# Kernel optimization log

Measured on AMD Instinct MI355X. Metric: run time of the kernel, lower is better.

Reference implementation:

```python
import jax, jax.numpy as jnp
import numpy as np

N, E, F_IN, F_HID, K = 100000, 1600000, 64, 64, 6


def setup_inputs() -> dict:
    key = jax.random.key(0)
    k1, k2, k3, k4, k5 = jax.random.split(key, 5)
    x = jax.random.normal(k1, (N, F_IN), dtype=jnp.float32)
    # edges with no self-loops (PyG ChebConv removes self loops before normalization)
    src = jax.random.randint(k2, (E,), 0, N, dtype=jnp.int32)
    off = jax.random.randint(k3, (E,), 1, N, dtype=jnp.int32)
    dst = (src + off) % N
    edge_index = jnp.stack([src, dst], axis=0)
    # Glorot-ish init for the K Chebyshev weight matrices
    W = jax.random.normal(k4, (K, F_IN, F_HID), dtype=jnp.float32) * (1.0 / np.sqrt(F_IN))
    b = jax.random.normal(k5, (F_HID,), dtype=jnp.float32) * 0.01
    return {"x": x, "edge_index": edge_index, "W": W, "b": b}


def reference(x, edge_index, W, b):
    # ChebConv with sym normalization, lambda_max = 2.0 (PyG default):
    # scaled Laplacian L_hat = 2*L/lambda_max - I = -D^{-1/2} A D^{-1/2} (zero diagonal)
    row = edge_index[0].astype(jnp.int32)  # source j
    col = edge_index[1].astype(jnp.int32)  # target i
    n = x.shape[0]
    deg = jax.ops.segment_sum(jnp.ones_like(row, dtype=x.dtype), row, num_segments=n)
    dinv = jnp.where(deg > 0, jax.lax.rsqrt(deg), jnp.zeros_like(deg))
    w = -(dinv[row] * dinv[col])  # [E] edge weights of L_hat

    def prop(h):  # h: [N, F] -> L_hat @ h via gather-scale-scatter
        return jax.ops.segment_sum(w[:, None] * h[row], col, num_segments=n)

    # Chebyshev recurrence: Tx_0 = x, Tx_1 = L_hat x, Tx_k = 2 L_hat Tx_{k-1} - Tx_{k-2}
    Tx0 = x
    out = Tx0 @ W[0]
    Tx1 = prop(Tx0)
    out = out + Tx1 @ W[1]
    for k in range(2, W.shape[0]):
        Tx2 = 2.0 * prop(Tx1) - Tx0
        out = out + Tx2 @ W[k]
        Tx0, Tx1 = Tx1, Tx2
    return jax.nn.relu(out + b)
```

## Files before the change

kernel.cpp:

```cpp
#include <hip/hip_runtime.h>


constexpr int F = 64;
constexpr int SCAN_ELEMS = 1024;
constexpr int BSH = 9;
constexpr int EPB = 2048;
constexpr int PNPW = 8;

typedef __attribute__((ext_vector_type(8))) short short8;
typedef __attribute__((ext_vector_type(4))) float floatx4;
typedef __attribute__((ext_vector_type(2))) float floatx2;

#if defined(__has_builtin)
#if __has_builtin(__builtin_amdgcn_cvt_pk_f32_fp8) && __has_builtin(__builtin_amdgcn_cvt_pk_fp8_f32)
#define HAVE_FP8 1
#endif
#endif
#ifndef HAVE_FP8
#define HAVE_FP8 0
#endif

__device__ __forceinline__ unsigned short f_to_bf(float f) {
    unsigned u = __float_as_uint(f);
    u += 0x7FFFu + ((u >> 16) & 1u);
    return (unsigned short)(u >> 16);
}
__device__ __forceinline__ float bf_to_f(unsigned short s) {
    return __uint_as_float(((unsigned)s) << 16);
}
__device__ __forceinline__ float4 bf4_to_f4(ushort4 u) {
    float4 f;
    f.x = bf_to_f(u.x); f.y = bf_to_f(u.y); f.z = bf_to_f(u.z); f.w = bf_to_f(u.w);
    return f;
}

#if HAVE_FP8
__device__ __forceinline__ float4 fp8x4_to_f4(unsigned u) {
    floatx2 lo = __builtin_amdgcn_cvt_pk_f32_fp8((int)u, false);
    floatx2 hi = __builtin_amdgcn_cvt_pk_f32_fp8((int)u, true);
    float4 f;
    f.x = lo.x; f.y = lo.y; f.z = hi.x; f.w = hi.y;
    return f;
}
__device__ __forceinline__ unsigned f4_to_fp8x4(float a, float b, float c, float d) {
    int pk = 0;
    pk = __builtin_amdgcn_cvt_pk_fp8_f32(a, b, pk, false);
    pk = __builtin_amdgcn_cvt_pk_fp8_f32(c, d, pk, true);
    return (unsigned)pk;
}
#else
__device__ __forceinline__ float4 fp8x4_to_f4(unsigned u) { return make_float4(0, 0, 0, 0); }
__device__ __forceinline__ unsigned f4_to_fp8x4(float a, float b, float c, float d) { return 0; }
#endif

__global__ void hist2_kernel(const int* __restrict__ row, const int* __restrict__ col,
                             int* __restrict__ gcH, int* __restrict__ gcS,
                             int P, int G, int E) {
    __shared__ int hH[256], hS[256];
    const int tid = threadIdx.x, blk = blockIdx.x;
    hH[tid] = 0; hS[tid] = 0;
    __syncthreads();
    const int start = blk * EPB + tid * 8;
    if (start + 7 < E) {
        const int4 c0 = *(const int4*)(col + start);
        const int4 c1 = *(const int4*)(col + start + 4);
        const int4 r0 = *(const int4*)(row + start);
        const int4 r1 = *(const int4*)(row + start + 4);
        atomicAdd(&hH[c0.x >> BSH], 1); atomicAdd(&hH[c0.y >> BSH], 1);
        atomicAdd(&hH[c0.z >> BSH], 1); atomicAdd(&hH[c0.w >> BSH], 1);
        atomicAdd(&hH[c1.x >> BSH], 1); atomicAdd(&hH[c1.y >> BSH], 1);
        atomicAdd(&hH[c1.z >> BSH], 1); atomicAdd(&hH[c1.w >> BSH], 1);
        atomicAdd(&hS[r0.x >> BSH], 1); atomicAdd(&hS[r0.y >> BSH], 1);
        atomicAdd(&hS[r0.z >> BSH], 1); atomicAdd(&hS[r0.w >> BSH], 1);
        atomicAdd(&hS[r1.x >> BSH], 1); atomicAdd(&hS[r1.y >> BSH], 1);
        atomicAdd(&hS[r1.z >> BSH], 1); atomicAdd(&hS[r1.w >> BSH], 1);
    } else {
        for (int k = start; k < E && k < start + 8; ++k) {
            atomicAdd(&hH[col[k] >> BSH], 1);
            atomicAdd(&hS[row[k] >> BSH], 1);
        }
    }
    __syncthreads();
    if (tid < P) {
        gcH[(size_t)tid * G + blk] = hH[tid];
        gcS[(size_t)tid * G + blk] = hS[tid];
    }
}

__device__ __forceinline__ int4 load_cnt4(const int* __restrict__ cnt, int i, int N) {
    int4 v = make_int4(0, 0, 0, 0);
    if (i + 3 < N) {
        v = *(const int4*)(cnt + i);
    } else {
        if (i + 0 < N) v.x = cnt[i + 0];
        if (i + 1 < N) v.y = cnt[i + 1];
        if (i + 2 < N) v.z = cnt[i + 2];
        if (i + 3 < N) v.w = cnt[i + 3];
    }
    return v;
}

__global__ void scan1_kernel(const int* __restrict__ cnt, int* __restrict__ bsum, int N) {
    const int tid = threadIdx.x;
    const int i = blockIdx.x * SCAN_ELEMS + tid * 4;
    int4 v = load_cnt4(cnt, i, N);
    int s = v.x + v.y + v.z + v.w;
#pragma unroll
    for (int off = 1; off < 64; off <<= 1) s += __shfl_xor(s, off);
    __shared__ int ws[4];
    if ((tid & 63) == 0) ws[tid >> 6] = s;
    __syncthreads();
    if (tid == 0) bsum[blockIdx.x] = ws[0] + ws[1] + ws[2] + ws[3];
}

__global__ void scan2_kernel(const int* __restrict__ bsum, int* __restrict__ boff,
                             int* __restrict__ total_out, int nb) {
    const int tid = threadIdx.x;
    const int lane = tid & 63, w = tid >> 6;
    int v = (tid < nb) ? bsum[tid] : 0;
    int inc = v;
#pragma unroll
    for (int off = 1; off < 64; off <<= 1) {
        int t = __shfl_up(inc, off);
        if (lane >= off) inc += t;
    }
    __shared__ int wsum[4];
    if (lane == 63) wsum[w] = inc;
    __syncthreads();
    int wo = 0;
    for (int k = 0; k < w; ++k) wo += wsum[k];
    const int excl = wo + inc - v;
    if (tid < nb) boff[tid] = excl;
    if (tid == nb - 1) *total_out = excl + v;
}

__global__ void scan3_kernel(const int* __restrict__ cnt, const int* __restrict__ boff,
                             int* __restrict__ dst, int N) {
    const int tid = threadIdx.x;
    const int lane = tid & 63, w = tid >> 6;
    const int i = blockIdx.x * SCAN_ELEMS + tid * 4;
    int4 v = load_cnt4(cnt, i, N);
    const int s = v.x + v.y + v.z + v.w;
    int inc = s;
#pragma unroll
    for (int off = 1; off < 64; off <<= 1) {
        int t = __shfl_up(inc, off);
        if (lane >= off) inc += t;
    }
    __shared__ int wsum[4];
    if (lane == 63) wsum[w] = inc;
    __syncthreads();
    int wo = 0;
    for (int k = 0; k < w; ++k) wo += wsum[k];
    const int r0 = boff[blockIdx.x] + wo + inc - s;
    const int r1 = r0 + v.x, r2 = r1 + v.y, r3 = r2 + v.z;
    if (i + 3 < N) {
        *(int4*)(dst + i) = make_int4(r0, r1, r2, r3);
    } else {
        if (i + 0 < N) dst[i + 0] = r0;
        if (i + 1 < N) dst[i + 1] = r1;
        if (i + 2 < N) dst[i + 2] = r2;
        if (i + 3 < N) dst[i + 3] = r3;
    }
}

__global__ void part2_kernel(const int* __restrict__ row, const int* __restrict__ col,
                             const int* __restrict__ goH, const int* __restrict__ goS,
                             int* __restrict__ partH, int* __restrict__ partS,
                             int P, int G, int E) {
    __shared__ int cH[256], cS[256];
    const int tid = threadIdx.x, blk = blockIdx.x;
    if (tid < P) {
        cH[tid] = goH[(size_t)tid * G + blk];
        cS[tid] = goS[(size_t)tid * G + blk];
    }
    __syncthreads();
    const int start = blk * EPB + tid * 8;
    for (int k = start; k < E && k < start + 8; ++k) {
        const int c = col[k], r = row[k];
        const int posH = atomicAdd(&cH[c >> BSH], 1);
        partH[posH] = ((c & ((1 << BSH) - 1)) << 23) | r;
        const int posS = atomicAdd(&cS[r >> BSH], 1);
        partS[posS] = r;
    }
}

__global__ void bucketC_kernel(const int* __restrict__ part, const int* __restrict__ goff,
                               int* __restrict__ rowptr, int* __restrict__ csr,
                               int P, int G, int N, int E) {
    __shared__ int cnt[512];
    __shared__ int excl[512];
    __shared__ int wsum[4];
    const int tid = threadIdx.x;
    const int b = blockIdx.x;
    const int base_node = b << BSH;
    const int nn = min(512, N - base_node);
    const int estart = goff[(size_t)b * G];
    const int eend = (b + 1 < P) ? goff[(size_t)(b + 1) * G] : E;

    cnt[tid] = 0; cnt[tid + 256] = 0;
    __syncthreads();
    for (int i = estart + tid; i < eend; i += 256)
        atomicAdd(&cnt[((unsigned)part[i]) >> 23], 1);
    __syncthreads();
    {
        const int lane = tid & 63, w = tid >> 6;
        const int a0 = cnt[2 * tid], a1 = cnt[2 * tid + 1];
        const int ps = a0 + a1;
        int inc = ps;
#pragma unroll
        for (int off = 1; off < 64; off <<= 1) {
            int t = __shfl_up(inc, off);
            if (lane >= off) inc += t;
        }
        if (lane == 63) wsum[w] = inc;
        __syncthreads();
        int wo = 0;
        for (int k = 0; k < w; ++k) wo += wsum[k];
        const int ep = wo + inc - ps;
        excl[2 * tid] = ep;
        excl[2 * tid + 1] = ep + a0;
    }
    __syncthreads();
    if (tid < nn) rowptr[base_node + tid] = estart + excl[tid];
    for (int ln = 256 + tid; ln < nn; ln += 256) rowptr[base_node + ln] = estart + excl[ln];
    if (b == P - 1 && tid == 0) rowptr[N] = E;
    cnt[tid] = 0; cnt[tid + 256] = 0;
    __syncthreads();
    for (int i = estart + tid; i < eend; i += 256) {
        const int pk = part[i];
        const int ln = ((unsigned)pk) >> 23;
        const int pos = atomicAdd(&cnt[ln], 1);
        csr[estart + excl[ln] + pos] = pk & 0x7FFFFF;
    }
}

__global__ void bucketD_kernel(const int* __restrict__ partS, const int* __restrict__ goffS,
                               float* __restrict__ dinv, float* __restrict__ dinv2,
                               float* __restrict__ rdinv, int P, int G, int N, int E) {
    __shared__ int cnt[512];
    const int tid = threadIdx.x;
    const int b = blockIdx.x;
    const int base_node = b << BSH;
    const int nn = min(512, N - base_node);
    const int estart = goffS[(size_t)b * G];
    const int eend = (b + 1 < P) ? goffS[(size_t)(b + 1) * G] : E;
    cnt[tid] = 0; cnt[tid + 256] = 0;
    __syncthreads();
    for (int i = estart + tid; i < eend; i += 256)
        atomicAdd(&cnt[partS[i] - base_node], 1);
    __syncthreads();
    for (int l = tid; l < nn; l += 256) {
        const int dI = cnt[l];
        const float d = (float)dI;
        const bool ok = dI > 0;
        dinv[base_node + l]  = ok ? rsqrtf(d) : 0.0f;
        dinv2[base_node + l] = ok ? 1.0f / d : 0.0f;
        rdinv[base_node + l] = ok ? sqrtf(d) : 0.0f;
    }
}

__global__ void init_s0_kernel(const float* __restrict__ dinv, const float* __restrict__ x,
                               unsigned short* __restrict__ S0b, unsigned char* __restrict__ S0f8,
                               int NF, int write8) {
    int i = blockIdx.x * blockDim.x + threadIdx.x;
    int j = i * 4;
    if (j >= NF) return;
    const float dv = dinv[j >> 6];
    const float4 v = *(const float4*)(x + j);
    const float a = dv * v.x, bb = dv * v.y, c = dv * v.z, d = dv * v.w;
    ushort4 u;
    u.x = f_to_bf(a); u.y = f_to_bf(bb); u.z = f_to_bf(c); u.w = f_to_bf(d);
    *(ushort4*)(S0b + j) = u;
    if (write8) *(unsigned*)(S0f8 + j) = f4_to_fp8x4(a, bb, c, d);
}

template <int FIRST>
__global__ __launch_bounds__(256, 6)
void prop_g4(const int* __restrict__ rowptr, const int* __restrict__ csr,
             const float* __restrict__ dinv2, const unsigned short* __restrict__ Sprev,
             const unsigned short* __restrict__ Sm2, unsigned short* __restrict__ Sk, int N) {
    const int lane = threadIdx.x & 63;
    const int g16 = lane & 48;
    const int fl = lane & 15;
    const int wave = threadIdx.x >> 6;
    const int wbase = (blockIdx.x * 4 + wave) * PNPW;
    for (int j = 0; j < PNPW; j += 4) {
        const int n = wbase + j + (g16 >> 4);
        const bool nv = n < N;
        const int nc = nv ? n : N - 1;
        const int s = rowptr[nc], e = rowptr[nc + 1];
        const int len = e - s;
        float4 acc = {0.f, 0.f, 0.f, 0.f};
        for (int c = 0; c < len; c += 16) {
            const int ii = s + c + fl;
            const int idxv = csr[ii < e ? ii : e - 1];
            const int mm = min(16, len - c);
            ushort4 u[16];
#pragma unroll
            for (int t = 0; t < 16; ++t) {
                const int it = __shfl(idxv, g16 + t);
                u[t] = *(const ushort4*)(Sprev + (size_t)it * F + fl * 4);
            }
#pragma unroll
            for (int t = 0; t < 16; ++t) {
                if (t < mm) {
                    const float4 v = bf4_to_f4(u[t]);
                    acc.x += v.x; acc.y += v.y; acc.z += v.z; acc.w += v.w;
                }
            }
        }
        if (nv) {
            const float d2 = dinv2[n];
            float4 sn;
            if (FIRST) {
                sn.x = -d2 * acc.x; sn.y = -d2 * acc.y;
                sn.z = -d2 * acc.z; sn.w = -d2 * acc.w;
            } else {
                const float4 m2 = bf4_to_f4(*(const ushort4*)(Sm2 + (size_t)n * F + fl * 4));
                sn.x = -2.f * d2 * acc.x - m2.x; sn.y = -2.f * d2 * acc.y - m2.y;
                sn.z = -2.f * d2 * acc.z - m2.z; sn.w = -2.f * d2 * acc.w - m2.w;
            }
            ushort4 o;
            o.x = f_to_bf(sn.x); o.y = f_to_bf(sn.y);
            o.z = f_to_bf(sn.z); o.w = f_to_bf(sn.w);
            *(ushort4*)(Sk + (size_t)n * F + fl * 4) = o;
        }
    }
}

template <int FIRST, int W8>
__global__ __launch_bounds__(256, 6)
void prop_f8(const int* __restrict__ rowptr, const int* __restrict__ csr,
             const float* __restrict__ dinv2, const unsigned char* __restrict__ S8prev,
             const unsigned short* __restrict__ Sm2, unsigned short* __restrict__ Sk,
             unsigned char* __restrict__ Sk8, int N) {
    const int lane = threadIdx.x & 63;
    const int g16 = lane & 48;
    const int fl = lane & 15;
    const int wave = threadIdx.x >> 6;
    const int wbase = (blockIdx.x * 4 + wave) * PNPW;
    for (int j = 0; j < PNPW; j += 4) {
        const int n = wbase + j + (g16 >> 4);
        const bool nv = n < N;
        const int nc = nv ? n : N - 1;
        const int s = rowptr[nc], e = rowptr[nc + 1];
        const int len = e - s;
        float4 acc = {0.f, 0.f, 0.f, 0.f};
        for (int c = 0; c < len; c += 16) {
            const int ii = s + c + fl;
            const int idxv = csr[ii < e ? ii : e - 1];
            const int mm = min(16, len - c);
            unsigned u[16];
#pragma unroll
            for (int t = 0; t < 16; ++t) {
                const int it = __shfl(idxv, g16 + t);
                u[t] = *(const unsigned*)(S8prev + (size_t)it * F + fl * 4);
            }
#pragma unroll
            for (int t = 0; t < 16; ++t) {
                if (t < mm) {
                    const float4 v = fp8x4_to_f4(u[t]);
                    acc.x += v.x; acc.y += v.y; acc.z += v.z; acc.w += v.w;
                }
            }
        }
        if (nv) {
            const float d2 = dinv2[n];
            float4 sn;
            if (FIRST) {
                sn.x = -d2 * acc.x; sn.y = -d2 * acc.y;
                sn.z = -d2 * acc.z; sn.w = -d2 * acc.w;
            } else {
                const float4 m2 = bf4_to_f4(*(const ushort4*)(Sm2 + (size_t)n * F + fl * 4));
                sn.x = -2.f * d2 * acc.x - m2.x; sn.y = -2.f * d2 * acc.y - m2.y;
                sn.z = -2.f * d2 * acc.z - m2.z; sn.w = -2.f * d2 * acc.w - m2.w;
            }
            ushort4 o;
            o.x = f_to_bf(sn.x); o.y = f_to_bf(sn.y);
            o.z = f_to_bf(sn.z); o.w = f_to_bf(sn.w);
            *(ushort4*)(Sk + (size_t)n * F + fl * 4) = o;
            if (W8) *(unsigned*)(Sk8 + (size_t)n * F + fl * 4) = f4_to_fp8x4(sn.x, sn.y, sn.z, sn.w);
        }
    }
}

__global__ void wfrag_kernel(const float* __restrict__ W, unsigned short* __restrict__ Wfrag) {
    const int idx = blockIdx.x * blockDim.x + threadIdx.x;
    if (idx >= 4 * 12 * 64) return;
    const int lane = idx & 63;
    const int s = (idx >> 6) % 12;
    const int ft = idx / (64 * 12);
    const int n = ft * 16 + (lane & 15);
    const int quad = lane >> 4;
    unsigned short v[8];
#pragma unroll
    for (int j = 0; j < 8; ++j) {
        const int kg = s * 32 + quad * 8 + j;
        const int kk = kg >> 6, f = kg & 63;
        v[j] = f_to_bf(W[kk * F * F + f * F + n]);
    }
    ushort4 lo = {v[0], v[1], v[2], v[3]};
    ushort4 hi = {v[4], v[5], v[6], v[7]};
    *(ushort4*)(Wfrag + (size_t)idx * 8) = lo;
    *(ushort4*)(Wfrag + (size_t)idx * 8 + 4) = hi;
}

__global__ __launch_bounds__(256, 3)
void mfma_out_kernel(const float* __restrict__ x, const unsigned short* __restrict__ Sstack,
                     const unsigned short* __restrict__ Wfrag, const float* __restrict__ rdinv,
                     const float* __restrict__ dinv2, const float* __restrict__ W,
                     const float* __restrict__ b, float* __restrict__ out, int N, int NF) {
    const int lane = threadIdx.x & 63;
    const int wave = threadIdx.x >> 6;
    const int quad = lane >> 4;
    const int fl = lane & 15;
    const int tm = (blockIdx.x * 4 + wave) * 16;
    if (tm >= N) return;
    const int ma = tm + fl;
    const int mac = ma < N ? ma : N - 1;

    const unsigned short* sa = Sstack + (size_t)mac * F + quad * 8;

    short8 Afr[12];
#pragma unroll
    for (int s = 0; s < 12; ++s) {
        const int kk = s >> 1, f0 = (s & 1) * 32;
        Afr[s] = *(const short8*)(sa + (size_t)kk * NF + f0);
    }

    floatx4 C0 = {0.f, 0.f, 0.f, 0.f};
    floatx4 C1 = {0.f, 0.f, 0.f, 0.f};
    floatx4 C2 = {0.f, 0.f, 0.f, 0.f};
    floatx4 C3 = {0.f, 0.f, 0.f, 0.f};
    const unsigned short* wf = Wfrag + (size_t)lane * 8;
#pragma unroll
    for (int s = 0; s < 12; ++s) {
        const short8 B0 = *(const short8*)(wf + (size_t)(0 * 12 + s) * 64 * 8);
        const short8 B1 = *(const short8*)(wf + (size_t)(1 * 12 + s) * 64 * 8);
        const short8 B2 = *(const short8*)(wf + (size_t)(2 * 12 + s) * 64 * 8);
        const short8 B3 = *(const short8*)(wf + (size_t)(3 * 12 + s) * 64 * 8);
        C0 = __builtin_amdgcn_mfma_f32_16x16x32_bf16(Afr[s], B0, C0, 0, 0, 0);
        C1 = __builtin_amdgcn_mfma_f32_16x16x32_bf16(Afr[s], B1, C1, 0, 0, 0);
        C2 = __builtin_amdgcn_mfma_f32_16x16x32_bf16(Afr[s], B2, C2, 0, 0, 0);
        C3 = __builtin_amdgcn_mfma_f32_16x16x32_bf16(Afr[s], B3, C3, 0, 0, 0);
    }

    const float bl0 = b[0 * 16 + fl];
    const float bl1 = b[1 * 16 + fl];
    const float bl2 = b[2 * 16 + fl];
    const float bl3 = b[3 * 16 + fl];

#pragma unroll
    for (int r = 0; r < 4; ++r) {
        const int m = tm + quad * 4 + r;
        if (m >= N) continue;
        const float rs = rdinv[m];
        const bool z = (dinv2[m] == 0.0f);
        float v0 = rs * C0[r], v1 = rs * C1[r], v2 = rs * C2[r], v3 = rs * C3[r];
        if (z) {
            const float* xr = x + (size_t)m * F;
            float f0 = 0.f, f1 = 0.f, f2 = 0.f, f3 = 0.f;
            for (int f = 0; f < F; ++f) {
                const float xv = xr[f];
                const float* w0 = W + 0 * F * F + f * F;
                const float* w2 = W + 2 * F * F + f * F;
                const float* w4 = W + 4 * F * F + f * F;
                f0 += xv * (w0[0 * 16 + fl] - w2[0 * 16 + fl] + w4[0 * 16 + fl]);
                f1 += xv * (w0[1 * 16 + fl] - w2[1 * 16 + fl] + w4[1 * 16 + fl]);
                f2 += xv * (w0[2 * 16 + fl] - w2[2 * 16 + fl] + w4[2 * 16 + fl]);
                f3 += xv * (w0[3 * 16 + fl] - w2[3 * 16 + fl] + w4[3 * 16 + fl]);
            }
            v0 = f0; v1 = f1; v2 = f2; v3 = f3;
        }
        float* orow = out + (size_t)m * F;
        orow[0 * 16 + fl] = fmaxf(v0 + bl0, 0.f);
        orow[1 * 16 + fl] = fmaxf(v1 + bl1, 0.f);
        orow[2 * 16 + fl] = fmaxf(v2 + bl2, 0.f);
        orow[3 * 16 + fl] = fmaxf(v3 + bl3, 0.f);
    }
}

extern "C" void kernel_launch(void* const* d_in, const int* in_sizes, int n_in,
                              void* d_out, int out_size, void* d_ws, size_t ws_size,
                              hipStream_t stream) {
    const float* x = (const float*)d_in[0];
    const int* ei = (const int*)d_in[1];
    const float* W = (const float*)d_in[2];
    const float* b = (const float*)d_in[3];

    const int N = in_sizes[0] / F;
    const int E = in_sizes[1] / 2;
    const int NF = N * F;
    const int* row = ei;
    const int* col = ei + E;

    const int P = (N + 511) >> BSH;
    const int G = (E + EPB - 1) / EPB;
    const int M = P * G;

    char* p = (char*)d_ws;
    auto alloc = [&](size_t bytes) {
        char* r = p;
        p += (bytes + 63) & ~(size_t)63;
        return r;
    };
    float* dinv   = (float*)alloc((size_t)N * sizeof(float));
    float* dinv2  = (float*)alloc((size_t)N * sizeof(float));
    float* rdinv  = (float*)alloc((size_t)N * sizeof(float));
    int*   rowptr = (int*)alloc((size_t)(N + 1) * sizeof(int));
    int*   bsum   = (int*)alloc(256 * sizeof(int));
    int*   boff   = (int*)alloc(256 * sizeof(int));
    int*   totS   = (int*)alloc(64);
    int*   gcH    = (int*)alloc((size_t)M * sizeof(int));
    int*   goH    = (int*)alloc((size_t)M * sizeof(int));
    int*   gcS    = (int*)alloc((size_t)M * sizeof(int));
    int*   goS    = (int*)alloc((size_t)M * sizeof(int));
    int*   csr    = (int*)alloc((size_t)E * sizeof(int));
    unsigned short* Sstack = (unsigned short*)alloc((size_t)6 * NF * sizeof(unsigned short));
    unsigned short* Wfrag  = (unsigned short*)alloc((size_t)4 * 12 * 64 * 8 * sizeof(unsigned short));
    unsigned char* F8A = (unsigned char*)alloc((size_t)NF);
    unsigned char* F8B = (unsigned char*)alloc((size_t)NF);
    const size_t needed = (size_t)(p - (char*)d_ws);
    const bool pathA = HAVE_FP8 && ws_size >= needed;
    int* partH = (int*)Sstack;
    int* partS = (int*)(Sstack + (size_t)NF);
    float* out = (float*)d_out;

    const int B = 256;
    const int nsbM = (M + SCAN_ELEMS - 1) / SCAN_ELEMS;
    const int pgrid = (N + 4 * PNPW - 1) / (4 * PNPW);

    hist2_kernel<<<G, B, 0, stream>>>(row, col, gcH, gcS, P, G, E);
    scan1_kernel<<<nsbM, B, 0, stream>>>(gcH, bsum, M);
    scan2_kernel<<<1, B, 0, stream>>>(bsum, boff, rowptr + N, nsbM);
    scan3_kernel<<<nsbM, B, 0, stream>>>(gcH, boff, goH, M);
    scan1_kernel<<<nsbM, B, 0, stream>>>(gcS, bsum, M);
    scan2_kernel<<<1, B, 0, stream>>>(bsum, boff, totS, nsbM);
    scan3_kernel<<<nsbM, B, 0, stream>>>(gcS, boff, goS, M);
    part2_kernel<<<G, B, 0, stream>>>(row, col, goH, goS, partH, partS, P, G, E);
    bucketC_kernel<<<P, B, 0, stream>>>(partH, goH, rowptr, csr, P, G, N, E);
    bucketD_kernel<<<P, B, 0, stream>>>(partS, goS, dinv, dinv2, rdinv, P, G, N, E);

    wfrag_kernel<<<(4 * 12 * 64 + B - 1) / B, B, 0, stream>>>(W, Wfrag);
    init_s0_kernel<<<(NF / 4 + B - 1) / B, B, 0, stream>>>(dinv, x, Sstack, F8A, NF,
                                                           pathA ? 1 : 0);
    unsigned short* S1 = Sstack + (size_t)1 * NF;
    unsigned short* S2 = Sstack + (size_t)2 * NF;
    unsigned short* S3 = Sstack + (size_t)3 * NF;
    unsigned short* S4 = Sstack + (size_t)4 * NF;
    unsigned short* S5 = Sstack + (size_t)5 * NF;
    if (pathA) {
        prop_f8<1, 1><<<pgrid, B, 0, stream>>>(rowptr, csr, dinv2, F8A, Sstack, S1, F8B, N);
        prop_f8<0, 1><<<pgrid, B, 0, stream>>>(rowptr, csr, dinv2, F8B, Sstack, S2, F8A, N);
        prop_f8<0, 1><<<pgrid, B, 0, stream>>>(rowptr, csr, dinv2, F8A, S1, S3, F8B, N);
        prop_f8<0, 1><<<pgrid, B, 0, stream>>>(rowptr, csr, dinv2, F8B, S2, S4, F8A, N);
        prop_f8<0, 0><<<pgrid, B, 0, stream>>>(rowptr, csr, dinv2, F8A, S3, S5, F8B, N);
    } else {
        prop_g4<1><<<pgrid, B, 0, stream>>>(rowptr, csr, dinv2, Sstack, Sstack, S1, N);
        prop_g4<0><<<pgrid, B, 0, stream>>>(rowptr, csr, dinv2, S1, Sstack, S2, N);
        prop_g4<0><<<pgrid, B, 0, stream>>>(rowptr, csr, dinv2, S2, S1, S3, N);
        prop_g4<0><<<pgrid, B, 0, stream>>>(rowptr, csr, dinv2, S3, S2, S4, N);
        prop_g4<0><<<pgrid, B, 0, stream>>>(rowptr, csr, dinv2, S4, S3, S5, N);
    }
    mfma_out_kernel<<<(N + 63) / 64, 256, 0, stream>>>(x, Sstack, Wfrag, rdinv, dinv2,
                                                       W, b, out, N, NF);
}
```

Baseline: 368.0 us.

## Merge graph preprocessing kernels and drop the FP8 propagation path

Several preprocessing stages are merged into fewer launches. The two histogram scans now run as one scan over a combined count array, the two bucket kernels become one launch, and the weight-fragment build is fused with the first feature scaling. The edge-partition loop now uses vectorized loads, and the output kernel uses nontemporal loads and stores. The FP8 gather path is removed, so all five propagation steps gather bf16 features. That cuts launch and sync overhead in the setup phase but doubles the bytes gathered per neighbour in the dominant propagation kernels.

```diff
diff --git a/kernel.cpp b/kernel.cpp
--- a/kernel.cpp
+++ b/kernel.cpp
@@ -2,23 +2,14 @@
 
 
 constexpr int F = 64;
-constexpr int SCAN_ELEMS = 1024;
+constexpr int SCAN_ELEMS = 2048;
 constexpr int BSH = 9;
 constexpr int EPB = 2048;
 constexpr int PNPW = 8;
+constexpr int WFRAG_BLOCKS = 12;
 
 typedef __attribute__((ext_vector_type(8))) short short8;
 typedef __attribute__((ext_vector_type(4))) float floatx4;
-typedef __attribute__((ext_vector_type(2))) float floatx2;
-
-#if defined(__has_builtin)
-#if __has_builtin(__builtin_amdgcn_cvt_pk_f32_fp8) && __has_builtin(__builtin_amdgcn_cvt_pk_fp8_f32)
-#define HAVE_FP8 1
-#endif
-#endif
-#ifndef HAVE_FP8
-#define HAVE_FP8 0
-#endif
 
 __device__ __forceinline__ unsigned short f_to_bf(float f) {
     unsigned u = __float_as_uint(f);
@@ -33,25 +24,6 @@
     f.x = bf_to_f(u.x); f.y = bf_to_f(u.y); f.z = bf_to_f(u.z); f.w = bf_to_f(u.w);
     return f;
 }
-
-#if HAVE_FP8
-__device__ __forceinline__ float4 fp8x4_to_f4(unsigned u) {
-    floatx2 lo = __builtin_amdgcn_cvt_pk_f32_fp8((int)u, false);
-    floatx2 hi = __builtin_amdgcn_cvt_pk_f32_fp8((int)u, true);
-    float4 f;
-    f.x = lo.x; f.y = lo.y; f.z = hi.x; f.w = hi.y;
-    return f;
-}
-__device__ __forceinline__ unsigned f4_to_fp8x4(float a, float b, float c, float d) {
-    int pk = 0;
-    pk = __builtin_amdgcn_cvt_pk_fp8_f32(a, b, pk, false);
-    pk = __builtin_amdgcn_cvt_pk_fp8_f32(c, d, pk, true);
-    return (unsigned)pk;
-}
-#else
-__device__ __forceinline__ float4 fp8x4_to_f4(unsigned u) { return make_float4(0, 0, 0, 0); }
-__device__ __forceinline__ unsigned f4_to_fp8x4(float a, float b, float c, float d) { return 0; }
-#endif
 
 __global__ void hist2_kernel(const int* __restrict__ row, const int* __restrict__ col,
                              int* __restrict__ gcH, int* __restrict__ gcS,
@@ -102,9 +74,10 @@
 
 __global__ void scan1_kernel(const int* __restrict__ cnt, int* __restrict__ bsum, int N) {
     const int tid = threadIdx.x;
-    const int i = blockIdx.x * SCAN_ELEMS + tid * 4;
-    int4 v = load_cnt4(cnt, i, N);
-    int s = v.x + v.y + v.z + v.w;
+    const int i = blockIdx.x * SCAN_ELEMS + tid * 8;
+    int4 va = load_cnt4(cnt, i, N);
+    int4 vb = load_cnt4(cnt, i + 4, N);
+    int s = va.x + va.y + va.z + va.w + vb.x + vb.y + vb.z + vb.w;
 #pragma unroll
     for (int off = 1; off < 64; off <<= 1) s += __shfl_xor(s, off);
     __shared__ int ws[4];
@@ -138,9 +111,10 @@
                              int* __restrict__ dst, int N) {
     const int tid = threadIdx.x;
     const int lane = tid & 63, w = tid >> 6;
-    const int i = blockIdx.x * SCAN_ELEMS + tid * 4;
-    int4 v = load_cnt4(cnt, i, N);
-    const int s = v.x + v.y + v.z + v.w;
+    const int i = blockIdx.x * SCAN_ELEMS + tid * 8;
+    int4 va = load_cnt4(cnt, i, N);
+    int4 vb = load_cnt4(cnt, i + 4, N);
+    const int s = va.x + va.y + va.z + va.w + vb.x + vb.y + vb.z + vb.w;
     int inc = s;
 #pragma unroll
     for (int off = 1; off < 64; off <<= 1) {
@@ -153,14 +127,21 @@
     int wo = 0;
     for (int k = 0; k < w; ++k) wo += wsum[k];
     const int r0 = boff[blockIdx.x] + wo + inc - s;
-    const int r1 = r0 + v.x, r2 = r1 + v.y, r3 = r2 + v.z;
+    const int r1 = r0 + va.x, r2 = r1 + va.y, r3 = r2 + va.z;
+    const int r4 = r3 + va.w, r5 = r4 + vb.x, r6 = r5 + vb.y, r7 = r6 + vb.z;
     if (i + 3 < N) {
         *(int4*)(dst + i) = make_int4(r0, r1, r2, r3);
     } else {
         if (i + 0 < N) dst[i + 0] = r0;
         if (i + 1 < N) dst[i + 1] = r1;
         if (i + 2 < N) dst[i + 2] = r2;
-        if (i + 3 < N) dst[i + 3] = r3;
+    }
+    if (i + 7 < N) {
+        *(int4*)(dst + i + 4) = make_int4(r4, r5, r6, r7);
+    } else {
+        if (i + 4 < N) dst[i + 4] = r4;
+        if (i + 5 < N) dst[i + 5] = r5;
+        if (i + 6 < N) dst[i + 6] = r6;
     }
 }
 
@@ -172,107 +153,145 @@
     const int tid = threadIdx.x, blk = blockIdx.x;
     if (tid < P) {
         cH[tid] = goH[(size_t)tid * G + blk];
-        cS[tid] = goS[(size_t)tid * G + blk];
+        cS[tid] = goS[(size_t)tid * G + blk] - E;
     }
     __syncthreads();
     const int start = blk * EPB + tid * 8;
-    for (int k = start; k < E && k < start + 8; ++k) {
-        const int c = col[k], r = row[k];
-        const int posH = atomicAdd(&cH[c >> BSH], 1);
-        partH[posH] = ((c & ((1 << BSH) - 1)) << 23) | r;
-        const int posS = atomicAdd(&cS[r >> BSH], 1);
-        partS[posS] = r;
-    }
-}
-
-__global__ void bucketC_kernel(const int* __restrict__ part, const int* __restrict__ goff,
-                               int* __restrict__ rowptr, int* __restrict__ csr,
-                               int P, int G, int N, int E) {
+    if (start + 7 < E) {
+        const int4 c0 = *(const int4*)(col + start);
+        const int4 c1 = *(const int4*)(col + start + 4);
+        const int4 r0 = *(const int4*)(row + start);
+        const int4 r1 = *(const int4*)(row + start + 4);
+#define P2_DO(c, r)                                              \
+        {                                                        \
+            const int posH = atomicAdd(&cH[(c) >> BSH], 1);      \
+            partH[posH] = (((c) & ((1 << BSH) - 1)) << 23) | (r);\
+            const int posS = atomicAdd(&cS[(r) >> BSH], 1);      \
+            partS[posS] = (r);                                   \
+        }
+        P2_DO(c0.x, r0.x) P2_DO(c0.y, r0.y) P2_DO(c0.z, r0.z) P2_DO(c0.w, r0.w)
+        P2_DO(c1.x, r1.x) P2_DO(c1.y, r1.y) P2_DO(c1.z, r1.z) P2_DO(c1.w, r1.w)
+#undef P2_DO
+    } else {
+        for (int k = start; k < E && k < start + 8; ++k) {
+            const int c = col[k], r = row[k];
+            const int posH = atomicAdd(&cH[c >> BSH], 1);
+            partH[posH] = ((c & ((1 << BSH) - 1)) << 23) | r;
+            const int posS = atomicAdd(&cS[r >> BSH], 1);
+            partS[posS] = r;
+        }
+    }
+}
+
+__global__ void bucketCD_kernel(const int* __restrict__ part, const int* __restrict__ goff,
+                                const int* __restrict__ partS, const int* __restrict__ goffS,
+                                int* __restrict__ rowptr, int* __restrict__ csr,
+                                float* __restrict__ dinv, float* __restrict__ dinv2,
+                                float* __restrict__ rdinv,
+                                int P, int G, int N, int E) {
     __shared__ int cnt[512];
     __shared__ int excl[512];
     __shared__ int wsum[4];
     const int tid = threadIdx.x;
-    const int b = blockIdx.x;
-    const int base_node = b << BSH;
-    const int nn = min(512, N - base_node);
-    const int estart = goff[(size_t)b * G];
-    const int eend = (b + 1 < P) ? goff[(size_t)(b + 1) * G] : E;
-
-    cnt[tid] = 0; cnt[tid + 256] = 0;
-    __syncthreads();
-    for (int i = estart + tid; i < eend; i += 256)
-        atomicAdd(&cnt[((unsigned)part[i]) >> 23], 1);
-    __syncthreads();
-    {
-        const int lane = tid & 63, w = tid >> 6;
-        const int a0 = cnt[2 * tid], a1 = cnt[2 * tid + 1];
-        const int ps = a0 + a1;
-        int inc = ps;
-#pragma unroll
-        for (int off = 1; off < 64; off <<= 1) {
-            int t = __shfl_up(inc, off);
-            if (lane >= off) inc += t;
-        }
-        if (lane == 63) wsum[w] = inc;
-        __syncthreads();
-        int wo = 0;
-        for (int k = 0; k < w; ++k) wo += wsum[k];
-        const int ep = wo + inc - ps;
-        excl[2 * tid] = ep;
-        excl[2 * tid + 1] = ep + a0;
-    }
-    __syncthreads();
-    if (tid < nn) rowptr[base_node + tid] = estart + excl[tid];
-    for (int ln = 256 + tid; ln < nn; ln += 256) rowptr[base_node + ln] = estart + excl[ln];
-    if (b == P - 1 && tid == 0) rowptr[N] = E;
-    cnt[tid] = 0; cnt[tid + 256] = 0;
-    __syncthreads();
-    for (int i = estart + tid; i < eend; i += 256) {
-        const int pk = part[i];
-        const int ln = ((unsigned)pk) >> 23;
-        const int pos = atomicAdd(&cnt[ln], 1);
-        csr[estart + excl[ln] + pos] = pk & 0x7FFFFF;
-    }
-}
-
-__global__ void bucketD_kernel(const int* __restrict__ partS, const int* __restrict__ goffS,
-                               float* __restrict__ dinv, float* __restrict__ dinv2,
-                               float* __restrict__ rdinv, int P, int G, int N, int E) {
-    __shared__ int cnt[512];
+    const int bb = blockIdx.x;
+    if (bb < P) {
+        const int b = bb;
+        const int base_node = b << BSH;
+        const int nn = min(512, N - base_node);
+        const int estart = goff[(size_t)b * G];
+        const int eend = (b + 1 < P) ? goff[(size_t)(b + 1) * G] : E;
+
+        cnt[tid] = 0; cnt[tid + 256] = 0;
+        __syncthreads();
+        for (int i = estart + tid; i < eend; i += 256)
+            atomicAdd(&cnt[((unsigned)part[i]) >> 23], 1);
+        __syncthreads();
+        {
+            const int lane = tid & 63, w = tid >> 6;
+            const int a0 = cnt[2 * tid], a1 = cnt[2 * tid + 1];
+            const int ps = a0 + a1;
+            int inc = ps;
+#pragma unroll
+            for (int off = 1; off < 64; off <<= 1) {
+                int t = __shfl_up(inc, off);
+                if (lane >= off) inc += t;
+            }
+            if (lane == 63) wsum[w] = inc;
+            __syncthreads();
+            int wo = 0;
+            for (int k = 0; k < w; ++k) wo += wsum[k];
+            const int ep = wo + inc - ps;
+            excl[2 * tid] = ep;
+            excl[2 * tid + 1] = ep + a0;
+        }
+        __syncthreads();
+        for (int ln = tid; ln < nn; ln += 256) rowptr[base_node + ln] = estart + excl[ln];
+        if (b == P - 1 && tid == 0) rowptr[N] = E;
+        cnt[tid] = 0; cnt[tid + 256] = 0;
+        __syncthreads();
+        for (int i = estart + tid; i < eend; i += 256) {
+            const int pk = part[i];
+            const int ln = ((unsigned)pk) >> 23;
+            const int pos = atomicAdd(&cnt[ln], 1);
+            csr[estart + excl[ln] + pos] = pk & 0x7FFFFF;
+        }
+    } else {
+        const int b = bb - P;
+        const int base_node = b << BSH;
+        const int nn = min(512, N - base_node);
+        const int estart = goffS[(size_t)b * G] - E;
+        const int eend = ((b + 1 < P) ? goffS[(size_t)(b + 1) * G] - E : E);
+        cnt[tid] = 0; cnt[tid + 256] = 0;
+        __syncthreads();
+        for (int i = estart + tid; i < eend; i += 256)
+            atomicAdd(&cnt[partS[i] - base_node], 1);
+        __syncthreads();
+        for (int l = tid; l < nn; l += 256) {
+            const int dI = cnt[l];
+            const float d = (float)dI;
+            const bool ok = dI > 0;
+            dinv[base_node + l]  = ok ? rsqrtf(d) : 0.0f;
+            dinv2[base_node + l] = ok ? 1.0f / d : 0.0f;
+            rdinv[base_node + l] = ok ? sqrtf(d) : 0.0f;
+        }
+    }
+}
+
+__global__ void init_ws0_kernel(const float* __restrict__ W, unsigned short* __restrict__ Wfrag,
+                                const float* __restrict__ dinv, const float* __restrict__ x,
+                                unsigned short* __restrict__ S0b, int NF) {
     const int tid = threadIdx.x;
-    const int b = blockIdx.x;
-    const int base_node = b << BSH;
-    const int nn = min(512, N - base_node);
-    const int estart = goffS[(size_t)b * G];
-    const int eend = (b + 1 < P) ? goffS[(size_t)(b + 1) * G] : E;
-    cnt[tid] = 0; cnt[tid + 256] = 0;
-    __syncthreads();
-    for (int i = estart + tid; i < eend; i += 256)
-        atomicAdd(&cnt[partS[i] - base_node], 1);
-    __syncthreads();
-    for (int l = tid; l < nn; l += 256) {
-        const int dI = cnt[l];
-        const float d = (float)dI;
-        const bool ok = dI > 0;
-        dinv[base_node + l]  = ok ? rsqrtf(d) : 0.0f;
-        dinv2[base_node + l] = ok ? 1.0f / d : 0.0f;
-        rdinv[base_node + l] = ok ? sqrtf(d) : 0.0f;
-    }
-}
-
-__global__ void init_s0_kernel(const float* __restrict__ dinv, const float* __restrict__ x,
-                               unsigned short* __restrict__ S0b, unsigned char* __restrict__ S0f8,
-                               int NF, int write8) {
-    int i = blockIdx.x * blockDim.x + threadIdx.x;
-    int j = i * 4;
-    if (j >= NF) return;
-    const float dv = dinv[j >> 6];
-    const float4 v = *(const float4*)(x + j);
-    const float a = dv * v.x, bb = dv * v.y, c = dv * v.z, d = dv * v.w;
-    ushort4 u;
-    u.x = f_to_bf(a); u.y = f_to_bf(bb); u.z = f_to_bf(c); u.w = f_to_bf(d);
-    *(ushort4*)(S0b + j) = u;
-    if (write8) *(unsigned*)(S0f8 + j) = f4_to_fp8x4(a, bb, c, d);
+    const int bid = blockIdx.x;
+    if (bid < WFRAG_BLOCKS) {
+        const int idx = bid * 256 + tid;
+        if (idx >= 4 * 12 * 64) return;
+        const int lane = idx & 63;
+        const int s = (idx >> 6) % 12;
+        const int ft = idx / (64 * 12);
+        const int n = ft * 16 + (lane & 15);
+        const int quad = lane >> 4;
+        unsigned short v[8];
+#pragma unroll
+        for (int j = 0; j < 8; ++j) {
+            const int kg = s * 32 + quad * 8 + j;
+            const int kk = kg >> 6, f = kg & 63;
+            v[j] = f_to_bf(W[kk * F * F + f * F + n]);
+        }
+        ushort4 lo = {v[0], v[1], v[2], v[3]};
+        ushort4 hi = {v[4], v[5], v[6], v[7]};
+        *(ushort4*)(Wfrag + (size_t)idx * 8) = lo;
+        *(ushort4*)(Wfrag + (size_t)idx * 8 + 4) = hi;
+    } else {
+        const int i = (bid - WFRAG_BLOCKS) * 256 + tid;
+        const int j = i * 4;
+        if (j >= NF) return;
+        const float dv = dinv[j >> 6];
+        const float4 v = *(const float4*)(x + j);
+        ushort4 u;
+        u.x = f_to_bf(dv * v.x); u.y = f_to_bf(dv * v.y);
+        u.z = f_to_bf(dv * v.z); u.w = f_to_bf(dv * v.w);
+        *(ushort4*)(S0b + j) = u;
+    }
 }
 
 template <int FIRST>
@@ -329,83 +348,6 @@
     }
 }
 
-template <int FIRST, int W8>
-__global__ __launch_bounds__(256, 6)
-void prop_f8(const int* __restrict__ rowptr, const int* __restrict__ csr,
-             const float* __restrict__ dinv2, const unsigned char* __restrict__ S8prev,
-             const unsigned short* __restrict__ Sm2, unsigned short* __restrict__ Sk,
-             unsigned char* __restrict__ Sk8, int N) {
-    const int lane = threadIdx.x & 63;
-    const int g16 = lane & 48;
-    const int fl = lane & 15;
-    const int wave = threadIdx.x >> 6;
-    const int wbase = (blockIdx.x * 4 + wave) * PNPW;
-    for (int j = 0; j < PNPW; j += 4) {
-        const int n = wbase + j + (g16 >> 4);
-        const bool nv = n < N;
-        const int nc = nv ? n : N - 1;
-        const int s = rowptr[nc], e = rowptr[nc + 1];
-        const int len = e - s;
-        float4 acc = {0.f, 0.f, 0.f, 0.f};
-        for (int c = 0; c < len; c += 16) {
-            const int ii = s + c + fl;
-            const int idxv = csr[ii < e ? ii : e - 1];
-            const int mm = min(16, len - c);
-            unsigned u[16];
-#pragma unroll
-            for (int t = 0; t < 16; ++t) {
-                const int it = __shfl(idxv, g16 + t);
-                u[t] = *(const unsigned*)(S8prev + (size_t)it * F + fl * 4);
-            }
-#pragma unroll
-            for (int t = 0; t < 16; ++t) {
-                if (t < mm) {
-                    const float4 v = fp8x4_to_f4(u[t]);
-                    acc.x += v.x; acc.y += v.y; acc.z += v.z; acc.w += v.w;
-                }
-            }
-        }
-        if (nv) {
-            const float d2 = dinv2[n];
-            float4 sn;
-            if (FIRST) {
-                sn.x = -d2 * acc.x; sn.y = -d2 * acc.y;
-                sn.z = -d2 * acc.z; sn.w = -d2 * acc.w;
-            } else {
-                const float4 m2 = bf4_to_f4(*(const ushort4*)(Sm2 + (size_t)n * F + fl * 4));
-                sn.x = -2.f * d2 * acc.x - m2.x; sn.y = -2.f * d2 * acc.y - m2.y;
-                sn.z = -2.f * d2 * acc.z - m2.z; sn.w = -2.f * d2 * acc.w - m2.w;
-            }
-            ushort4 o;
-            o.x = f_to_bf(sn.x); o.y = f_to_bf(sn.y);
-            o.z = f_to_bf(sn.z); o.w = f_to_bf(sn.w);
-            *(ushort4*)(Sk + (size_t)n * F + fl * 4) = o;
-            if (W8) *(unsigned*)(Sk8 + (size_t)n * F + fl * 4) = f4_to_fp8x4(sn.x, sn.y, sn.z, sn.w);
-        }
-    }
-}
-
-__global__ void wfrag_kernel(const float* __restrict__ W, unsigned short* __restrict__ Wfrag) {
-    const int idx = blockIdx.x * blockDim.x + threadIdx.x;
-    if (idx >= 4 * 12 * 64) return;
-    const int lane = idx & 63;
-    const int s = (idx >> 6) % 12;
-    const int ft = idx / (64 * 12);
-    const int n = ft * 16 + (lane & 15);
-    const int quad = lane >> 4;
-    unsigned short v[8];
-#pragma unroll
-    for (int j = 0; j < 8; ++j) {
-        const int kg = s * 32 + quad * 8 + j;
-        const int kk = kg >> 6, f = kg & 63;
-        v[j] = f_to_bf(W[kk * F * F + f * F + n]);
-    }
-    ushort4 lo = {v[0], v[1], v[2], v[3]};
-    ushort4 hi = {v[4], v[5], v[6], v[7]};
-    *(ushort4*)(Wfrag + (size_t)idx * 8) = lo;
-    *(ushort4*)(Wfrag + (size_t)idx * 8 + 4) = hi;
-}
-
 __global__ __launch_bounds__(256, 3)
 void mfma_out_kernel(const float* __restrict__ x, const unsigned short* __restrict__ Sstack,
                      const unsigned short* __restrict__ Wfrag, const float* __restrict__ rdinv,
@@ -426,7 +368,7 @@
 #pragma unroll
     for (int s = 0; s < 12; ++s) {
         const int kk = s >> 1, f0 = (s & 1) * 32;
-        Afr[s] = *(const short8*)(sa + (size_t)kk * NF + f0);
+        Afr[s] = __builtin_nontemporal_load((const short8*)(sa + (size_t)kk * NF + f0));
     }
 
     floatx4 C0 = {0.f, 0.f, 0.f, 0.f};
@@ -474,10 +416,10 @@
             v0 = f0; v1 = f1; v2 = f2; v3 = f3;
         }
         float* orow = out + (size_t)m * F;
-        orow[0 * 16 + fl] = fmaxf(v0 + bl0, 0.f);
-        orow[1 * 16 + fl] = fmaxf(v1 + bl1, 0.f);
-        orow[2 * 16 + fl] = fmaxf(v2 + bl2, 0.f);
-        orow[3 * 16 + fl] = fmaxf(v3 + bl3, 0.f);
+        __builtin_nontemporal_store(fmaxf(v0 + bl0, 0.f), orow + 0 * 16 + fl);
+        __builtin_nontemporal_store(fmaxf(v1 + bl1, 0.f), orow + 1 * 16 + fl);
+        __builtin_nontemporal_store(fmaxf(v2 + bl2, 0.f), orow + 2 * 16 + fl);
+        __builtin_nontemporal_store(fmaxf(v3 + bl3, 0.f), orow + 3 * 16 + fl);
     }
 }
 
@@ -498,6 +440,7 @@
     const int P = (N + 511) >> BSH;
     const int G = (E + EPB - 1) / EPB;
     const int M = P * G;
+    const int M2 = 2 * M;
 
     char* p = (char*)d_ws;
     auto alloc = [&](size_t bytes) {
@@ -512,57 +455,40 @@
     int*   bsum   = (int*)alloc(256 * sizeof(int));
     int*   boff   = (int*)alloc(256 * sizeof(int));
     int*   totS   = (int*)alloc(64);
-    int*   gcH    = (int*)alloc((size_t)M * sizeof(int));
-    int*   goH    = (int*)alloc((size_t)M * sizeof(int));
-    int*   gcS    = (int*)alloc((size_t)M * sizeof(int));
-    int*   goS    = (int*)alloc((size_t)M * sizeof(int));
+    int*   gc     = (int*)alloc((size_t)M2 * sizeof(int));
+    int*   go     = (int*)alloc((size_t)M2 * sizeof(int));
     int*   csr    = (int*)alloc((size_t)E * sizeof(int));
     unsigned short* Sstack = (unsigned short*)alloc((size_t)6 * NF * sizeof(unsigned short));
     unsigned short* Wfrag  = (unsigned short*)alloc((size_t)4 * 12 * 64 * 8 * sizeof(unsigned short));
-    unsigned char* F8A = (unsigned char*)alloc((size_t)NF);
-    unsigned char* F8B = (unsigned char*)alloc((size_t)NF);
-    const size_t needed = (size_t)(p - (char*)d_ws);
-    const bool pathA = HAVE_FP8 && ws_size >= needed;
     int* partH = (int*)Sstack;
     int* partS = (int*)(Sstack + (size_t)NF);
     float* out = (float*)d_out;
+    (void)ws_size;
 
     const int B = 256;
-    const int nsbM = (M + SCAN_ELEMS - 1) / SCAN_ELEMS;
+    const int nsb = (M2 + SCAN_ELEMS - 1) / SCAN_ELEMS;
     const int pgrid = (N + 4 * PNPW - 1) / (4 * PNPW);
-
-    hist2_kernel<<<G, B, 0, stream>>>(row, col, gcH, gcS, P, G, E);
-    scan1_kernel<<<nsbM, B, 0, stream>>>(gcH, bsum, M);
-    scan2_kernel<<<1, B, 0, stream>>>(bsum, boff, rowptr + N, nsbM);
-    scan3_kernel<<<nsbM, B, 0, stream>>>(gcH, boff, goH, M);
-    scan1_kernel<<<nsbM, B, 0, stream>>>(gcS, bsum, M);
-    scan2_kernel<<<1, B, 0, stream>>>(bsum, boff, totS, nsbM);
-    scan3_kernel<<<nsbM, B, 0, stream>>>(gcS, boff, goS, M);
-    part2_kernel<<<G, B, 0, stream>>>(row, col, goH, goS, partH, partS, P, G, E);
-    bucketC_kernel<<<P, B, 0, stream>>>(partH, goH, rowptr, csr, P, G, N, E);
-    bucketD_kernel<<<P, B, 0, stream>>>(partS, goS, dinv, dinv2, rdinv, P, G, N, E);
-
-    wfrag_kernel<<<(4 * 12 * 64 + B - 1) / B, B, 0, stream>>>(W, Wfrag);
-    init_s0_kernel<<<(NF / 4 + B - 1) / B, B, 0, stream>>>(dinv, x, Sstack, F8A, NF,
-                                                           pathA ? 1 : 0);
+    const int igrid = WFRAG_BLOCKS + (NF / 4 + B - 1) / B;
+
+    hist2_kernel<<<G, B, 0, stream>>>(row, col, gc, gc + M, P, G, E);
+    scan1_kernel<<<nsb, B, 0, stream>>>(gc, bsum, M2);
+    scan2_kernel<<<1, B, 0, stream>>>(bsum, boff, totS, nsb);
+    scan3_kernel<<<nsb, B, 0, stream>>>(gc, boff, go, M2);
+    part2_kernel<<<G, B, 0, stream>>>(row, col, go, go + M, partH, partS, P, G, E);
+    bucketCD_kernel<<<2 * P, B, 0, stream>>>(partH, go, partS, go + M, rowptr, csr,
+                                             dinv, dinv2, rdinv, P, G, N, E);
+    init_ws0_kernel<<<igrid, B, 0, stream>>>(W, Wfrag, dinv, x, Sstack, NF);
+
     unsigned short* S1 = Sstack + (size_t)1 * NF;
     unsigned short* S2 = Sstack + (size_t)2 * NF;
     unsigned short* S3 = Sstack + (size_t)3 * NF;
     unsigned short* S4 = Sstack + (size_t)4 * NF;
     unsigned short* S5 = Sstack + (size_t)5 * NF;
-    if (pathA) {
-        prop_f8<1, 1><<<pgrid, B, 0, stream>>>(rowptr, csr, dinv2, F8A, Sstack, S1, F8B, N);
-        prop_f8<0, 1><<<pgrid, B, 0, stream>>>(rowptr, csr, dinv2, F8B, Sstack, S2, F8A, N);
-        prop_f8<0, 1><<<pgrid, B, 0, stream>>>(rowptr, csr, dinv2, F8A, S1, S3, F8B, N);
-        prop_f8<0, 1><<<pgrid, B, 0, stream>>>(rowptr, csr, dinv2, F8B, S2, S4, F8A, N);
-        prop_f8<0, 0><<<pgrid, B, 0, stream>>>(rowptr, csr, dinv2, F8A, S3, S5, F8B, N);
-    } else {
-        prop_g4<1><<<pgrid, B, 0, stream>>>(rowptr, csr, dinv2, Sstack, Sstack, S1, N);
-        prop_g4<0><<<pgrid, B, 0, stream>>>(rowptr, csr, dinv2, S1, Sstack, S2, N);
-        prop_g4<0><<<pgrid, B, 0, stream>>>(rowptr, csr, dinv2, S2, S1, S3, N);
-        prop_g4<0><<<pgrid, B, 0, stream>>>(rowptr, csr, dinv2, S3, S2, S4, N);
-        prop_g4<0><<<pgrid, B, 0, stream>>>(rowptr, csr, dinv2, S4, S3, S5, N);
-    }
+    prop_g4<1><<<pgrid, B, 0, stream>>>(rowptr, csr, dinv2, Sstack, Sstack, S1, N);
+    prop_g4<0><<<pgrid, B, 0, stream>>>(rowptr, csr, dinv2, S1, Sstack, S2, N);
+    prop_g4<0><<<pgrid, B, 0, stream>>>(rowptr, csr, dinv2, S2, S1, S3, N);
+    prop_g4<0><<<pgrid, B, 0, stream>>>(rowptr, csr, dinv2, S3, S2, S4, N);
+    prop_g4<0><<<pgrid, B, 0, stream>>>(rowptr, csr, dinv2, S4, S3, S5, N);
     mfma_out_kernel<<<(N + 63) / 64, 256, 0, stream>>>(x, Sstack, Wfrag, rdinv, dinv2,
                                                        W, b, out, N, NF);
 }
```

Measured after the change: 338.1 us, median of 2. 1.09x faster.
